# Optimization experiments

Hardware: AMD Instinct MI355X
Metric: run time of the kernel (lower is better)

The kernel has to match this reference:

```python
import jax, jax.numpy as jnp
import numpy as np


def setup_inputs() -> dict:
    key = jax.random.key(0)
    ks = jax.random.split(key, 6)
    B, S, F, U = 64, 1024, 1024, 1024
    scale = 0.02
    return {
        "features": jax.random.normal(ks[0], (B, S, F), dtype=jnp.float32),
        "hidden": jax.random.normal(ks[1], (B, U), dtype=jnp.float32),
        "W1_w": jax.random.normal(ks[2], (F, U), dtype=jnp.float32) * scale,
        "W1_b": jnp.zeros((U,), dtype=jnp.float32),
        "W2_w": jax.random.normal(ks[3], (U, U), dtype=jnp.float32) * scale,
        "W2_b": jnp.zeros((U,), dtype=jnp.float32),
        "V_w": jax.random.normal(ks[4], (U, 1), dtype=jnp.float32) * scale,
        "V_b": jnp.zeros((1,), dtype=jnp.float32),
    }


def reference(features, hidden, W1_w, W1_b, W2_w, W2_b, V_w, V_b):
    # features: [B, S, F]; hidden: [B, H]
    # score = tanh(W1(features) + W2(hidden)[:, None, :])  -> [B, S, U]
    proj_f = jnp.einsum("bsf,fu->bsu", features, W1_w) + W1_b
    proj_h = hidden @ W2_w + W2_b  # [B, U]
    score = jnp.tanh(proj_f + proj_h[:, None, :])
    # logits: [B, S, 1]; softmax over seq axis (axis=1)
    logits = jnp.einsum("bsu,uo->bso", score, V_w) + V_b
    attention_weights = jax.nn.softmax(logits, axis=1)
    # context: sum over seq of weights * features -> [B, F]
    context_vector = jnp.sum(attention_weights * features, axis=1)
    return context_vector, attention_weights
```

## Files before the change

kernel.cpp:

```cpp
#include <hip/hip_runtime.h>
#include <hip/hip_bf16.h>
#include <stdint.h>

#define B_ 64
#define S_ 1024
#define F_ 1024
#define U_ 1024

typedef __attribute__((ext_vector_type(4))) float  f4;
typedef __attribute__((ext_vector_type(4))) float  f32x4;
typedef __attribute__((ext_vector_type(8))) short  short8;
typedef unsigned int u32;

static __device__ __forceinline__ short f2bf(float x){
    union { float f; uint32_t u; } v; v.f = x;
    uint32_t u = v.u;
    u += 0x7fffu + ((u >> 16) & 1u);
    return (short)(u >> 16);
}

static __device__ __forceinline__ void glds16(const void* g, void* l){
    __builtin_amdgcn_global_load_lds(
        (const __attribute__((address_space(1))) u32*)g,
        (__attribute__((address_space(3))) u32*)l, 16, 0, 0);
}

static __device__ __forceinline__ float fast_tanh(float x){
    float e = __expf(2.f * x);
    return 1.f - 2.f / (e + 1.f);
}

__global__ void pack_w1(const float* __restrict__ W1, short* __restrict__ Bws){
    int g = blockIdx.x * 256 + threadIdx.x;
    int n    =  g        & 127;
    int kgrp = (g >> 7)  & 3;
    int nb   = (g >> 9)  & 7;
    int kb   =  g >> 12;
    int u  = nb*128 + n;
    int f0 = kb*32 + kgrp*8;
    short8 o;
#pragma unroll
    for (int j = 0; j < 8; ++j)
        o[j] = f2bf(W1[(size_t)(f0 + j)*U_ + u]);
    *(short8*)&Bws[(size_t)g * 8] = o;
}

__global__ void pack_feat(const float* __restrict__ F, short* __restrict__ out){
    int bid = blockIdx.x;
    int t = threadIdx.x;
    int half = bid & 1, kt = (bid >> 1) & 31, mb = bid >> 6;
    int row = half*64 + (t >> 2);
    int kq  = t & 3;
    const float* src = F + (size_t)(mb*128 + row)*1024 + kt*32 + kq*8;
    f4 a = *(const f4*)src;
    f4 b = *(const f4*)(src + 4);
    short8 o;
    o[0]=f2bf(a[0]); o[1]=f2bf(a[1]); o[2]=f2bf(a[2]); o[3]=f2bf(a[3]);
    o[4]=f2bf(b[0]); o[5]=f2bf(b[1]); o[6]=f2bf(b[2]); o[7]=f2bf(b[3]);
    *(short8*)&out[(size_t)(mb*32 + kt)*4096 + (kq*128 + row)*8] = o;
}

__global__ void hb_kernel(const float* __restrict__ hidden, const float* __restrict__ W2,
                          const float* __restrict__ W2b, const float* __restrict__ W1b,
                          float* __restrict__ hb){
    __shared__ float hs[4][1024];
    int ub = blockIdx.x, bg = blockIdx.y, t = threadIdx.x;
    for (int i = t; i < 4096; i += 256) ((float*)hs)[i] = hidden[(size_t)bg*4096 + i];
    __syncthreads();
    int u = ub*256 + t;
    float base = W1b[u] + W2b[u];
    float a0 = 0.f, a1 = 0.f, a2 = 0.f, a3 = 0.f;
#pragma unroll 4
    for (int k = 0; k < 1024; ++k){
        float w = W2[(size_t)k*1024 + u];
        a0 = fmaf(hs[0][k], w, a0);
        a1 = fmaf(hs[1][k], w, a1);
        a2 = fmaf(hs[2][k], w, a2);
        a3 = fmaf(hs[3][k], w, a3);
    }
    hb[(size_t)(bg*4 + 0)*1024 + u] = base + a0;
    hb[(size_t)(bg*4 + 1)*1024 + u] = base + a1;
    hb[(size_t)(bg*4 + 2)*1024 + u] = base + a2;
    hb[(size_t)(bg*4 + 3)*1024 + u] = base + a3;
}

static __device__ __forceinline__ void swz_mbnb(int bid, int& mb, int& nb){
    int xcd = bid & 7;
    int seq = bid >> 3;
    nb = seq & 7;
    mb = xcd*64 + (seq >> 3);
}

__global__ __launch_bounds__(256) void gemm_v2(
        const short* __restrict__ Abf, const short* __restrict__ Bws,
        const float* __restrict__ hb, const float* __restrict__ Vw,
        float* __restrict__ logits){
    __shared__ short Ab[2][4096];
    __shared__ short Bb[2][4096];

    const int t = threadIdx.x;
    int mb, nb; swz_mbnb(blockIdx.x, mb, nb);
    const int m0 = mb*128, n0 = nb*128;
    const int batch = m0 >> 10;
    const int w = t >> 6, l = t & 63;
    const int wr = w >> 1, wc = w & 1;
    const int kg = l >> 4, fr = l & 15;

    const char* Asrc = (const char*)Abf + ((size_t)(mb*32) << 13) + (w<<11) + (l<<4);
    const char* Bsrc = (const char*)Bws + ((size_t)nb << 13) + (w<<11) + (l<<4);
    char* AdstBase[2] = { (char*)&Ab[0][0] + (w<<11), (char*)&Ab[1][0] + (w<<11) };
    char* BdstBase[2] = { (char*)&Bb[0][0] + (w<<11), (char*)&Bb[1][0] + (w<<11) };

#define STAGE(sel, kt) do{                                   \
        const char* as_ = Asrc + ((size_t)(kt) << 13);       \
        const char* bs_ = Bsrc + ((size_t)(kt) << 16);       \
        glds16(as_,        AdstBase[sel]);                   \
        glds16(as_ + 1024, AdstBase[sel] + 1024);            \
        glds16(bs_,        BdstBase[sel]);                   \
        glds16(bs_ + 1024, BdstBase[sel] + 1024);            \
    }while(0)

    f32x4 acc[4][4];
#pragma unroll
    for (int i = 0; i < 4; ++i)
#pragma unroll
        for (int j = 0; j < 4; ++j) acc[i][j] = (f32x4)0.f;

    STAGE(0, 0);
    asm volatile("s_waitcnt vmcnt(0)");
    __syncthreads();

    for (int kt = 0; kt < 32; ++kt){
        const int sel = kt & 1;
        if (kt < 31) STAGE(sel ^ 1, kt + 1);

        short8 af[4], bfr[4];
#pragma unroll
        for (int i = 0; i < 4; ++i)
            af[i] = *(const short8*)&Ab[sel][(kg*128 + wr*64 + i*16 + fr)*8];
#pragma unroll
        for (int j = 0; j < 4; ++j)
            bfr[j] = *(const short8*)&Bb[sel][(kg*128 + wc*64 + j*16 + fr)*8];
#pragma unroll
        for (int i = 0; i < 4; ++i)
#pragma unroll
            for (int j = 0; j < 4; ++j)
                acc[i][j] = __builtin_amdgcn_mfma_f32_16x16x32_bf16(af[i], bfr[j], acc[i][j], 0, 0, 0);
        __syncthreads();
    }
#undef STAGE

    float hv[4], vv[4];
#pragma unroll
    for (int j = 0; j < 4; ++j){
        int u = n0 + wc*64 + j*16 + fr;
        hv[j] = hb[batch*U_ + u];
        vv[j] = Vw[u];
    }
#pragma unroll
    for (int i = 0; i < 4; ++i){
#pragma unroll
        for (int reg = 0; reg < 4; ++reg){
            float sum = 0.f;
#pragma unroll
            for (int j = 0; j < 4; ++j){
                float sc = fast_tanh(acc[i][j][reg] + hv[j]);
                sum = fmaf(vv[j], sc, sum);
            }
            sum += __shfl_xor(sum, 1, 64);
            sum += __shfl_xor(sum, 2, 64);
            sum += __shfl_xor(sum, 4, 64);
            sum += __shfl_xor(sum, 8, 64);
            if (fr == 0)
                atomicAdd(&logits[m0 + wr*64 + i*16 + kg*4 + reg], sum);
        }
    }
}

__global__ __launch_bounds__(256) void gemm_fb(
        const float* __restrict__ A, const short* __restrict__ Bws,
        const float* __restrict__ hb, const float* __restrict__ Vw,
        float* __restrict__ logits){
    __shared__ short Abuf[4096];
    __shared__ short Bbuf[2][4096];

    const int t = threadIdx.x;
    int mb, nb; swz_mbnb(blockIdx.x, mb, nb);
    const int m0 = mb*128, n0 = nb*128;
    const int batch = m0 >> 10;
    const int w = t >> 6, l = t & 63;
    const int wr = w >> 1, wc = w & 1;
    const int kg = l >> 4, fr = l & 15;
    const int ar = t >> 1, ah = t & 1;

    const float* aptr = A + (size_t)(m0 + ar)*F_ + ah*16;

    f32x4 acc[4][4];
#pragma unroll
    for (int i = 0; i < 4; ++i)
#pragma unroll
        for (int j = 0; j < 4; ++j) acc[i][j] = (f32x4)0.f;

    f4 a0 = *(const f4*)(aptr + 0);
    f4 a1 = *(const f4*)(aptr + 4);
    f4 a2 = *(const f4*)(aptr + 8);
    f4 a3 = *(const f4*)(aptr + 12);
    {
        const char* src = (const char*)Bws + ((size_t)nb << 13) + (w<<11) + (l<<4);
        char* dst = (char*)&Bbuf[0][0] + (w<<11);
        glds16(src, dst);
        glds16(src + 1024, dst + 1024);
    }

    for (int kt = 0; kt < 32; ++kt){
        const int sel = kt & 1;
        short8 s0, s1;
        s0[0]=f2bf(a0[0]); s0[1]=f2bf(a0[1]); s0[2]=f2bf(a0[2]); s0[3]=f2bf(a0[3]);
        s0[4]=f2bf(a1[0]); s0[5]=f2bf(a1[1]); s0[6]=f2bf(a1[2]); s0[7]=f2bf(a1[3]);
        s1[0]=f2bf(a2[0]); s1[1]=f2bf(a2[1]); s1[2]=f2bf(a2[2]); s1[3]=f2bf(a2[3]);
        s1[4]=f2bf(a3[0]); s1[5]=f2bf(a3[1]); s1[6]=f2bf(a3[2]); s1[7]=f2bf(a3[3]);
        *(short8*)&Abuf[((2*ah+0)*128 + ar)*8] = s0;
        *(short8*)&Abuf[((2*ah+1)*128 + ar)*8] = s1;
        __syncthreads();

        if (kt < 31){
            const float* ap = aptr + (kt+1)*32;
            a0 = *(const f4*)(ap + 0);
            a1 = *(const f4*)(ap + 4);
            a2 = *(const f4*)(ap + 8);
            a3 = *(const f4*)(ap + 12);
            const char* src = (const char*)Bws + ((size_t)((kt+1)*8 + nb) << 13) + (w<<11) + (l<<4);
            char* dst = (char*)&Bbuf[sel^1][0] + (w<<11);
            glds16(src, dst);
            glds16(src + 1024, dst + 1024);
        }

        short8 af[4], bfr[4];
#pragma unroll
        for (int i = 0; i < 4; ++i)
            af[i] = *(const short8*)&Abuf[(kg*128 + wr*64 + i*16 + fr)*8];
#pragma unroll
        for (int j = 0; j < 4; ++j)
            bfr[j] = *(const short8*)&Bbuf[sel][(kg*128 + wc*64 + j*16 + fr)*8];
#pragma unroll
        for (int i = 0; i < 4; ++i)
#pragma unroll
            for (int j = 0; j < 4; ++j)
                acc[i][j] = __builtin_amdgcn_mfma_f32_16x16x32_bf16(af[i], bfr[j], acc[i][j], 0, 0, 0);
        __syncthreads();
    }

    float hv[4], vv[4];
#pragma unroll
    for (int j = 0; j < 4; ++j){
        int u = n0 + wc*64 + j*16 + fr;
        hv[j] = hb[batch*U_ + u];
        vv[j] = Vw[u];
    }
#pragma unroll
    for (int i = 0; i < 4; ++i){
#pragma unroll
        for (int reg = 0; reg < 4; ++reg){
            float sum = 0.f;
#pragma unroll
            for (int j = 0; j < 4; ++j){
                float sc = fast_tanh(acc[i][j][reg] + hv[j]);
                sum = fmaf(vv[j], sc, sum);
            }
            sum += __shfl_xor(sum, 1, 64);
            sum += __shfl_xor(sum, 2, 64);
            sum += __shfl_xor(sum, 4, 64);
            sum += __shfl_xor(sum, 8, 64);
            if (fr == 0)
                atomicAdd(&logits[m0 + wr*64 + i*16 + kg*4 + reg], sum);
        }
    }
}

__global__ void softmax_seq(float* __restrict__ lg){
    __shared__ float red[4], red2[4];
    int b = blockIdx.x, t = threadIdx.x;
    float v[4];
#pragma unroll
    for (int c = 0; c < 4; ++c) v[c] = lg[b*1024 + c*256 + t];
    float mx = fmaxf(fmaxf(v[0], v[1]), fmaxf(v[2], v[3]));
#pragma unroll
    for (int off = 32; off >= 1; off >>= 1) mx = fmaxf(mx, __shfl_xor(mx, off, 64));
    if ((t & 63) == 0) red[t >> 6] = mx;
    __syncthreads();
    mx = fmaxf(fmaxf(red[0], red[1]), fmaxf(red[2], red[3]));
    float e[4], s = 0.f;
#pragma unroll
    for (int c = 0; c < 4; ++c){ e[c] = __expf(v[c] - mx); s += e[c]; }
#pragma unroll
    for (int off = 32; off >= 1; off >>= 1) s += __shfl_xor(s, off, 64);
    if ((t & 63) == 0) red2[t >> 6] = s;
    __syncthreads();
    s = red2[0] + red2[1] + red2[2] + red2[3];
    float inv = 1.f / s;
#pragma unroll
    for (int c = 0; c < 4; ++c) lg[b*1024 + c*256 + t] = e[c] * inv;
}

__global__ void context_kernel(const float* __restrict__ feats, const float* __restrict__ wts,
                               float* __restrict__ ctx){
    __shared__ float wsh[128];
    int sh = blockIdx.x, b = blockIdx.y, t = threadIdx.x;
    if (t < 128) wsh[t] = wts[b*1024 + sh*128 + t];
    __syncthreads();
    const f4* fp = (const f4*)(feats + ((size_t)b*1024 + sh*128)*1024) + t;
    f4 a0 = (f4)0.f, a1 = (f4)0.f, a2 = (f4)0.f, a3 = (f4)0.f;
    for (int s = 0; s < 128; s += 4){
        a0 += wsh[s+0] * fp[(size_t)(s+0)*256];
        a1 += wsh[s+1] * fp[(size_t)(s+1)*256];
        a2 += wsh[s+2] * fp[(size_t)(s+2)*256];
        a3 += wsh[s+3] * fp[(size_t)(s+3)*256];
    }
    f4 r = (a0 + a1) + (a2 + a3);
    float* c = ctx + b*1024 + t*4;
    atomicAdd(c+0, r[0]); atomicAdd(c+1, r[1]);
    atomicAdd(c+2, r[2]); atomicAdd(c+3, r[3]);
}

extern "C" void kernel_launch(void* const* d_in, const int* in_sizes, int n_in,
                              void* d_out, int out_size, void* d_ws, size_t ws_size,
                              hipStream_t stream){
    const float* features = (const float*)d_in[0];
    const float* hidden   = (const float*)d_in[1];
    const float* W1w      = (const float*)d_in[2];
    const float* W1b      = (const float*)d_in[3];
    const float* W2w      = (const float*)d_in[4];
    const float* W2b      = (const float*)d_in[5];
    const float* Vw       = (const float*)d_in[6];

    float* out = (float*)d_out;
    float* ctx = out;
    float* att = out + 65536;

    short* Bws    = (short*)d_ws;
    float* hb     = (float*)((char*)d_ws + (size_t)2*1024*1024);
    short* featbf = (short*)((char*)d_ws + (size_t)2*1024*1024 + 256*1024);

    const size_t need = (size_t)2*1024*1024 + 256*1024 + (size_t)128*1024*1024;

    hipMemsetAsync(d_out, 0, (size_t)131072 * sizeof(float), stream);
    pack_w1<<<512, 256, 0, stream>>>(W1w, Bws);
    hb_kernel<<<dim3(4, 16), 256, 0, stream>>>(hidden, W2w, W2b, W1b, hb);

    if (ws_size >= need){
        pack_feat<<<32768, 256, 0, stream>>>(features, featbf);
        gemm_v2<<<4096, 256, 0, stream>>>(featbf, Bws, hb, Vw, att);
    } else {
        gemm_fb<<<4096, 256, 0, stream>>>(features, Bws, hb, Vw, att);
    }

    softmax_seq<<<64, 256, 0, stream>>>(att);
    context_kernel<<<dim3(8, 64), 256, 0, stream>>>(features, att, ctx);
}
```

Measured before the change: 762.1 us.

## Coalesce feature packing via LDS, split-K hidden projection, unroll GEMM double buffer

pack_feat now has each block load a full 128x32 tile with coalesced row-contiguous reads, transpose it through shared memory, and write it out with contiguous 16-byte stores. hb_kernel splits the K dimension four ways and accumulates with atomicAdd into a zeroed buffer, which raises parallelism for the small hidden projection. The GEMM main loop is unrolled by two with statically named LDS buffers so the compiler can resolve buffer addresses at compile time. The changes add a memset and atomics, and the split-K sum becomes order-dependent in float.

```diff
diff --git a/kernel.cpp b/kernel.cpp
--- a/kernel.cpp
+++ b/kernel.cpp
@@ -10,6 +10,7 @@
 typedef __attribute__((ext_vector_type(4))) float  f4;
 typedef __attribute__((ext_vector_type(4))) float  f32x4;
 typedef __attribute__((ext_vector_type(8))) short  short8;
+typedef __attribute__((ext_vector_type(4))) short  bf16x4;
 typedef unsigned int u32;
 
 static __device__ __forceinline__ short f2bf(float x){
@@ -45,43 +46,55 @@
     *(short8*)&Bws[(size_t)g * 8] = o;
 }
 
-__global__ void pack_feat(const float* __restrict__ F, short* __restrict__ out){
-    int bid = blockIdx.x;
-    int t = threadIdx.x;
-    int half = bid & 1, kt = (bid >> 1) & 31, mb = bid >> 6;
-    int row = half*64 + (t >> 2);
-    int kq  = t & 3;
-    const float* src = F + (size_t)(mb*128 + row)*1024 + kt*32 + kq*8;
-    f4 a = *(const f4*)src;
-    f4 b = *(const f4*)(src + 4);
-    short8 o;
-    o[0]=f2bf(a[0]); o[1]=f2bf(a[1]); o[2]=f2bf(a[2]); o[3]=f2bf(a[3]);
-    o[4]=f2bf(b[0]); o[5]=f2bf(b[1]); o[6]=f2bf(b[2]); o[7]=f2bf(b[3]);
-    *(short8*)&out[(size_t)(mb*32 + kt)*4096 + (kq*128 + row)*8] = o;
+__global__ __launch_bounds__(256) void pack_feat(const float* __restrict__ F,
+                                                 short* __restrict__ out){
+    __shared__ short tile[4096];
+    const int mb = blockIdx.x >> 5, kt = blockIdx.x & 31;
+    const int t = threadIdx.x;
+    const float* base = F + (size_t)mb*128*1024 + kt*32;
+#pragma unroll
+    for (int i = 0; i < 4; ++i){
+        int li = i*256 + t;
+        int row = li >> 3, c4 = li & 7;
+        f4 v = *(const f4*)(base + (size_t)row*1024 + c4*4);
+        bf16x4 s;
+        s[0]=f2bf(v[0]); s[1]=f2bf(v[1]); s[2]=f2bf(v[2]); s[3]=f2bf(v[3]);
+        int kgrp = c4 >> 1, half = c4 & 1;
+        *(bf16x4*)&tile[(kgrp*128 + row)*8 + half*4] = s;
+    }
+    __syncthreads();
+    short8* dst = (short8*)&out[(size_t)blockIdx.x * 4096];
+#pragma unroll
+    for (int i = 0; i < 2; ++i){
+        int e = i*256 + t;
+        dst[e] = *(const short8*)&tile[e*8];
+    }
 }
 
 __global__ void hb_kernel(const float* __restrict__ hidden, const float* __restrict__ W2,
                           const float* __restrict__ W2b, const float* __restrict__ W1b,
                           float* __restrict__ hb){
-    __shared__ float hs[4][1024];
-    int ub = blockIdx.x, bg = blockIdx.y, t = threadIdx.x;
-    for (int i = t; i < 4096; i += 256) ((float*)hs)[i] = hidden[(size_t)bg*4096 + i];
-    __syncthreads();
-    int u = ub*256 + t;
-    float base = W1b[u] + W2b[u];
-    float a0 = 0.f, a1 = 0.f, a2 = 0.f, a3 = 0.f;
+    __shared__ float hs[4][256];
+    const int ub = blockIdx.x, kc = blockIdx.y, bg = blockIdx.z, t = threadIdx.x;
+    for (int i = t; i < 1024; i += 256)
+        hs[i>>8][i&255] = hidden[(size_t)(bg*4 + (i>>8))*1024 + kc*256 + (i&255)];
+    __syncthreads();
+    const int u = ub*256 + t;
+    const float* w2 = W2 + (size_t)(kc*256)*1024 + u;
+    float a0=0.f, a1=0.f, a2=0.f, a3=0.f;
 #pragma unroll 4
-    for (int k = 0; k < 1024; ++k){
-        float w = W2[(size_t)k*1024 + u];
+    for (int k = 0; k < 256; ++k){
+        float w = w2[(size_t)k*1024];
         a0 = fmaf(hs[0][k], w, a0);
         a1 = fmaf(hs[1][k], w, a1);
         a2 = fmaf(hs[2][k], w, a2);
         a3 = fmaf(hs[3][k], w, a3);
     }
-    hb[(size_t)(bg*4 + 0)*1024 + u] = base + a0;
-    hb[(size_t)(bg*4 + 1)*1024 + u] = base + a1;
-    hb[(size_t)(bg*4 + 2)*1024 + u] = base + a2;
-    hb[(size_t)(bg*4 + 3)*1024 + u] = base + a3;
+    float base = (kc == 0) ? (W1b[u] + W2b[u]) : 0.f;
+    atomicAdd(&hb[(size_t)(bg*4+0)*1024 + u], base + a0);
+    atomicAdd(&hb[(size_t)(bg*4+1)*1024 + u], base + a1);
+    atomicAdd(&hb[(size_t)(bg*4+2)*1024 + u], base + a2);
+    atomicAdd(&hb[(size_t)(bg*4+3)*1024 + u], base + a3);
 }
 
 static __device__ __forceinline__ void swz_mbnb(int bid, int& mb, int& nb){
@@ -95,8 +108,8 @@
         const short* __restrict__ Abf, const short* __restrict__ Bws,
         const float* __restrict__ hb, const float* __restrict__ Vw,
         float* __restrict__ logits){
-    __shared__ short Ab[2][4096];
-    __shared__ short Bb[2][4096];
+    __shared__ short Ab0[4096], Ab1[4096];
+    __shared__ short Bb0[4096], Bb1[4096];
 
     const int t = threadIdx.x;
     int mb, nb; swz_mbnb(blockIdx.x, mb, nb);
@@ -108,16 +121,32 @@
 
     const char* Asrc = (const char*)Abf + ((size_t)(mb*32) << 13) + (w<<11) + (l<<4);
     const char* Bsrc = (const char*)Bws + ((size_t)nb << 13) + (w<<11) + (l<<4);
-    char* AdstBase[2] = { (char*)&Ab[0][0] + (w<<11), (char*)&Ab[1][0] + (w<<11) };
-    char* BdstBase[2] = { (char*)&Bb[0][0] + (w<<11), (char*)&Bb[1][0] + (w<<11) };
-
-#define STAGE(sel, kt) do{                                   \
+    char* Adst0 = (char*)Ab0 + (w<<11);  char* Adst1 = (char*)Ab1 + (w<<11);
+    char* Bdst0 = (char*)Bb0 + (w<<11);  char* Bdst1 = (char*)Bb1 + (w<<11);
+
+#define STAGE(D, kt) do{                                     \
         const char* as_ = Asrc + ((size_t)(kt) << 13);       \
         const char* bs_ = Bsrc + ((size_t)(kt) << 16);       \
-        glds16(as_,        AdstBase[sel]);                   \
-        glds16(as_ + 1024, AdstBase[sel] + 1024);            \
-        glds16(bs_,        BdstBase[sel]);                   \
-        glds16(bs_ + 1024, BdstBase[sel] + 1024);            \
+        glds16(as_,        Adst##D);                         \
+        glds16(as_ + 1024, Adst##D + 1024);                  \
+        glds16(bs_,        Bdst##D);                         \
+        glds16(bs_ + 1024, Bdst##D + 1024);                  \
+    }while(0)
+
+#define COMPUTE(AB, BB) do{                                                   \
+        short8 af[4], bfr[4];                                                 \
+        _Pragma("unroll")                                                     \
+        for (int i = 0; i < 4; ++i)                                           \
+            af[i] = *(const short8*)&AB[(kg*128 + wr*64 + i*16 + fr)*8];      \
+        _Pragma("unroll")                                                     \
+        for (int j = 0; j < 4; ++j)                                           \
+            bfr[j] = *(const short8*)&BB[(kg*128 + wc*64 + j*16 + fr)*8];     \
+        _Pragma("unroll")                                                     \
+        for (int i = 0; i < 4; ++i)                                           \
+            _Pragma("unroll")                                                 \
+            for (int j = 0; j < 4; ++j)                                       \
+                acc[i][j] = __builtin_amdgcn_mfma_f32_16x16x32_bf16(          \
+                                af[i], bfr[j], acc[i][j], 0, 0, 0);           \
     }while(0)
 
     f32x4 acc[4][4];
@@ -130,25 +159,16 @@
     asm volatile("s_waitcnt vmcnt(0)");
     __syncthreads();
 
-    for (int kt = 0; kt < 32; ++kt){
-        const int sel = kt & 1;
-        if (kt < 31) STAGE(sel ^ 1, kt + 1);
-
-        short8 af[4], bfr[4];
-#pragma unroll
-        for (int i = 0; i < 4; ++i)
-            af[i] = *(const short8*)&Ab[sel][(kg*128 + wr*64 + i*16 + fr)*8];
-#pragma unroll
-        for (int j = 0; j < 4; ++j)
-            bfr[j] = *(const short8*)&Bb[sel][(kg*128 + wc*64 + j*16 + fr)*8];
-#pragma unroll
-        for (int i = 0; i < 4; ++i)
-#pragma unroll
-            for (int j = 0; j < 4; ++j)
-                acc[i][j] = __builtin_amdgcn_mfma_f32_16x16x32_bf16(af[i], bfr[j], acc[i][j], 0, 0, 0);
+    for (int kt = 0; kt < 32; kt += 2){
+        STAGE(1, kt + 1);
+        COMPUTE(Ab0, Bb0);
         __syncthreads();
+        if (kt + 2 < 32) STAGE(0, kt + 2);
+        COMPUTE(Ab1, Bb1);
+        __syncthreads();
     }
 #undef STAGE
+#undef COMPUTE
 
     float hv[4], vv[4];
 #pragma unroll
@@ -343,12 +363,13 @@
 
     const size_t need = (size_t)2*1024*1024 + 256*1024 + (size_t)128*1024*1024;
 
-    hipMemsetAsync(d_out, 0, (size_t)131072 * sizeof(float), stream);
+    (void)hipMemsetAsync(d_out, 0, (size_t)131072 * sizeof(float), stream);
+    (void)hipMemsetAsync(hb, 0, (size_t)65536 * sizeof(float), stream);
     pack_w1<<<512, 256, 0, stream>>>(W1w, Bws);
-    hb_kernel<<<dim3(4, 16), 256, 0, stream>>>(hidden, W2w, W2b, W1b, hb);
+    hb_kernel<<<dim3(4, 4, 16), 256, 0, stream>>>(hidden, W2w, W2b, W1b, hb);
 
     if (ws_size >= need){
-        pack_feat<<<32768, 256, 0, stream>>>(features, featbf);
+        pack_feat<<<16384, 256, 0, stream>>>(features, featbf);
         gemm_v2<<<4096, 256, 0, stream>>>(featbf, Bws, hb, Vw, att);
     } else {
         gemm_fb<<<4096, 256, 0, stream>>>(features, Bws, hb, Vw, att);
```

New measurement: 674.7 us. -11.5%, faster.
